# Performance work log

Measured on AMD Instinct MI355X. Metric: run time of the kernel, lower is better.

The kernel has to match this reference:

```python
import jax, jax.numpy as jnp
import numpy as np

N0, N1, N2 = 200000, 50000, 10000
E0, E1 = 800000, 160000
IN_DIM, H1, H2, EMB = 256, 256, 256, 128


def gcn_layer(h_src, src_idx, dst_idx, n_src, n_dst, W, b):
    # DGL GraphConv, norm='both': D_dst^{-1/2} A D_src^{-1/2} X W + b,
    # degrees clamped to min 1 (allow_zero_in_degree=True -> zero rows stay zero).
    ones = jnp.ones(src_idx.shape[0], dtype=h_src.dtype)
    out_deg = jnp.clip(jax.ops.segment_sum(ones, src_idx, num_segments=n_src), 1.0)
    in_deg = jnp.clip(jax.ops.segment_sum(ones, dst_idx, num_segments=n_dst), 1.0)
    # in_dim >= out_dim here, so DGL multiplies by W first then aggregates;
    # result is identical either way.
    h = (h_src * jax.lax.rsqrt(out_deg)[:, None]) @ W          # [n_src, out]
    agg = jax.ops.segment_sum(h[src_idx], dst_idx, num_segments=n_dst)  # [n_dst, out]
    return agg * jax.lax.rsqrt(in_deg)[:, None] + b


def setup_inputs() -> dict:
    key = jax.random.key(0)
    ks = jax.random.split(key, 10)
    h = jax.random.normal(ks[0], (N0, IN_DIM), dtype=jnp.float32)
    src0 = jax.random.randint(ks[1], (E0,), 0, N0, dtype=jnp.int32)
    dst0 = jax.random.randint(ks[2], (E0,), 0, N1, dtype=jnp.int32)
    src1 = jax.random.randint(ks[3], (E1,), 0, N1, dtype=jnp.int32)
    dst1 = jax.random.randint(ks[4], (E1,), 0, N2, dtype=jnp.int32)
    s1 = 1.0 / np.sqrt(IN_DIM)
    s2 = 1.0 / np.sqrt(H1)
    sp = 1.0 / np.sqrt(H2)
    W1 = jax.random.normal(ks[5], (IN_DIM, H1), dtype=jnp.float32) * s1
    W2 = jax.random.normal(ks[6], (H1, H2), dtype=jnp.float32) * s2
    Wp = jax.random.normal(ks[7], (H2, EMB), dtype=jnp.float32) * sp
    b1 = jnp.zeros((H1,), dtype=jnp.float32)
    b2 = jnp.zeros((H2,), dtype=jnp.float32)
    bp = jnp.zeros((EMB,), dtype=jnp.float32)
    return {"h": h, "src0": src0, "dst0": dst0, "src1": src1, "dst1": dst1,
            "W1": W1, "b1": b1, "W2": W2, "b2": b2, "Wp": Wp, "bp": bp}


def reference(h, src0, dst0, src1, dst1, W1, b1, W2, b2, Wp, bp):
    h = gcn_layer(h, src0, dst0, N0, N1, W1, b1)   # [N1, H1]
    h = gcn_layer(h, src1, dst1, N1, N2, W2, b2)   # [N2, H2]
    return h @ Wp + bp                             # [N2, EMB]
```

## Files before the change

### kernel.cpp

```cpp
#include <hip/hip_runtime.h>
#include <cstddef>

#define N0 200000
#define N1 50000
#define N2 10000
#define E0 800000
#define E1 160000

typedef short bf16x8 __attribute__((ext_vector_type(8)));
typedef float f32x4 __attribute__((ext_vector_type(4)));
typedef unsigned short us8 __attribute__((ext_vector_type(8)));

__device__ __forceinline__ unsigned short f2bf(float f) {
    unsigned int u = __float_as_uint(f);
    unsigned int r = (u + 0x7FFF + ((u >> 16) & 1)) >> 16;
    return (unsigned short)r;
}
__device__ __forceinline__ float bf2f(unsigned short s) {
    return __uint_as_float(((unsigned int)s) << 16);
}

__global__ void pack_all(const float* __restrict__ W1, const float* __restrict__ W2,
                         const float* __restrict__ Wp,
                         unsigned short* __restrict__ W1p, unsigned short* __restrict__ W2p,
                         unsigned short* __restrict__ Wpp) {
    int tid = blockIdx.x * 256 + threadIdx.x;
    if (tid >= 320 * 64) return;
    int lane = tid & 63;
    int tile = tid >> 6;
    const float* W; unsigned short* Bp; int N; int lt;
    if (tile < 128)      { W = W1; Bp = W1p; N = 256; lt = tile; }
    else if (tile < 256) { W = W2; Bp = W2p; N = 256; lt = tile - 128; }
    else                 { W = Wp; Bp = Wpp; N = 128; lt = tile - 256; }
    int s  = lt & 7;
    int ct = lt >> 3;
    int col = ct * 16 + (lane & 15);
    int k0  = s * 32 + (lane >> 4) * 8;
    unsigned short* dst = Bp + ((size_t)lt * 64 + lane) * 8;
#pragma unroll
    for (int j = 0; j < 8; j++) dst[j] = f2bf(W[(size_t)(k0 + j) * N + col]);
}

__global__ void count_all(const int* __restrict__ src0, const int* __restrict__ dst0,
                          const int* __restrict__ src1, const int* __restrict__ dst1,
                          int* __restrict__ cnt_out0, int* __restrict__ cnt_in0,
                          int* __restrict__ cnt_out1, int* __restrict__ cnt_in1,
                          int* __restrict__ rank0, int* __restrict__ rank1) {
    int e = blockIdx.x * 256 + threadIdx.x;
    if (e < E0) {
        atomicAdd(&cnt_out0[src0[e]], 1);
        rank0[e] = atomicAdd(&cnt_in0[dst0[e]], 1);
    } else if (e < E0 + E1) {
        int f = e - E0;
        atomicAdd(&cnt_out1[src1[f]], 1);
        rank1[f] = atomicAdd(&cnt_in1[dst1[f]], 1);
    }
}

__global__ __launch_bounds__(256) void prescale_bf16(const float* __restrict__ H,
                                                     const int* __restrict__ cnt_out,
                                                     unsigned short* __restrict__ hsb) {
    const long long total = (long long)N0 * 32;
    const long long stride = (long long)gridDim.x * 256;
    for (long long g = (long long)blockIdx.x * 256 + threadIdx.x; g < total; g += stride) {
        int row = (int)(g >> 5);
        float rs = rsqrtf((float)max(cnt_out[row], 1));
        const float* p = H + g * 8;
        float4 x = *(const float4*)p;
        float4 y = *(const float4*)(p + 4);
        us8 o;
        o[0] = f2bf(x.x * rs); o[1] = f2bf(x.y * rs); o[2] = f2bf(x.z * rs); o[3] = f2bf(x.w * rs);
        o[4] = f2bf(y.x * rs); o[5] = f2bf(y.y * rs); o[6] = f2bf(y.z * rs); o[7] = f2bf(y.w * rs);
        *(us8*)(hsb + g * 8) = o;
    }
}

__global__ void scales_kernel(const int* __restrict__ cnt, float* __restrict__ rs, int n) {
    int i = blockIdx.x * 256 + threadIdx.x;
    if (i < n) rs[i] = rsqrtf((float)max(cnt[i], 1));
}

__global__ __launch_bounds__(1024) void scan2(const int* __restrict__ cnt_in0, int* __restrict__ rowptr0,
                                              const int* __restrict__ cnt_in1, int* __restrict__ rowptr1) {
    const int* cnt = blockIdx.x ? cnt_in1 : cnt_in0;
    int* rowptr    = blockIdx.x ? rowptr1 : rowptr0;
    const int n    = blockIdx.x ? N2 : N1;
    __shared__ int partial[1024];
    const int t = threadIdx.x;
    const int chunk = (n + 1023) / 1024;
    const int begin = t * chunk;
    const int end = min(begin + chunk, n);
    int sum = 0;
    for (int i = begin; i < end; i++) sum += cnt[i];
    partial[t] = sum;
    __syncthreads();
    for (int off = 1; off < 1024; off <<= 1) {
        int v = (t >= off) ? partial[t - off] : 0;
        __syncthreads();
        partial[t] += v;
        __syncthreads();
    }
    int run = partial[t] - sum;
    for (int i = begin; i < end; i++) {
        rowptr[i] = run;
        run += cnt[i];
    }
    if (t == 1023) rowptr[n] = partial[1023];
}

__global__ void fill_all(const int* __restrict__ src0, const int* __restrict__ dst0,
                         const int* __restrict__ src1, const int* __restrict__ dst1,
                         const int* __restrict__ rank0, const int* __restrict__ rank1,
                         const int* __restrict__ rowptr0, const int* __restrict__ rowptr1,
                         int* __restrict__ csr0, int* __restrict__ csr1) {
    int e = blockIdx.x * 256 + threadIdx.x;
    if (e < E0) {
        csr0[rowptr0[dst0[e]] + rank0[e]] = src0[e];
    } else if (e < E0 + E1) {
        int f = e - E0;
        csr1[rowptr1[dst1[f]] + rank1[f]] = src1[f];
    }
}

template <int NT, bool AF32, bool OBF16, bool BS>
__global__ __launch_bounds__(256) void gemm_mfma(const void* __restrict__ A_,
                                                 const unsigned short* __restrict__ Bp,
                                                 const float* __restrict__ rs,
                                                 const float* __restrict__ bias,
                                                 void* __restrict__ C_, int M, int N) {
    const int lane = threadIdx.x & 63;
    const int wave = threadIdx.x >> 6;
    const int rowBase = blockIdx.x * 64 + wave * 16;
    const int lm = lane & 15;
    const int quad = lane >> 4;

    f32x4 acc[NT];
#pragma unroll
    for (int ct = 0; ct < NT; ct++) acc[ct] = (f32x4){0.f, 0.f, 0.f, 0.f};

    const int rowA = min(rowBase + lm, M - 1);
    const float* af32 = (const float*)A_ + (size_t)rowA * 256 + quad * 8;
    const unsigned short* abf = (const unsigned short*)A_ + (size_t)rowA * 256 + quad * 8;

#pragma unroll 2
    for (int s = 0; s < 8; s++) {
        bf16x8 afrag;
        if (AF32) {
            float4 x = *(const float4*)(af32 + s * 32);
            float4 y = *(const float4*)(af32 + s * 32 + 4);
            union { unsigned short u[8]; bf16x8 v; } af;
            af.u[0] = f2bf(x.x); af.u[1] = f2bf(x.y); af.u[2] = f2bf(x.z); af.u[3] = f2bf(x.w);
            af.u[4] = f2bf(y.x); af.u[5] = f2bf(y.y); af.u[6] = f2bf(y.z); af.u[7] = f2bf(y.w);
            afrag = af.v;
        } else {
            afrag = *(const bf16x8*)(abf + s * 32);
        }
#pragma unroll
        for (int ct = 0; ct < NT; ct++) {
            bf16x8 bfrag = *(const bf16x8*)(Bp + (((size_t)ct * 8 + s) * 64 + lane) * 8);
            acc[ct] = __builtin_amdgcn_mfma_f32_16x16x32_bf16(afrag, bfrag, acc[ct], 0, 0, 0);
        }
    }

    f32x4 rsv = (f32x4){1.f, 1.f, 1.f, 1.f};
    if (rs) rsv = *(const f32x4*)(rs + min(rowBase + quad * 4, M - 4));
#pragma unroll
    for (int ct = 0; ct < NT; ct++) {
        int col = ct * 16 + lm;
        float bv = bias ? bias[col] : 0.0f;
#pragma unroll
        for (int i = 0; i < 4; i++) {
            int row = rowBase + quad * 4 + i;
            if (row < M) {
                float v = acc[ct][i];
                if (BS) { v = (v + bv) * rsv[i]; }
                else    { v = v * rsv[i] + bv; }
                if (OBF16) ((unsigned short*)C_)[(size_t)row * N + col] = f2bf(v);
                else       ((float*)C_)[(size_t)row * N + col] = v;
            }
        }
    }
}

__global__ __launch_bounds__(256) void gather_bf16(const unsigned short* __restrict__ Y,
                                                   const int* __restrict__ rowptr,
                                                   const int* __restrict__ csr,
                                                   const float* __restrict__ rs_dst,
                                                   const float* __restrict__ bias,
                                                   unsigned short* __restrict__ outb, int n_dst) {
    int w    = (blockIdx.x * 256 + threadIdx.x) >> 6;
    int lane = threadIdx.x & 63;
    if (w >= n_dst) return;
    int half = lane >> 5;
    int l32  = lane & 31;
    int e   = rowptr[w];
    int end = rowptr[w + 1];
    float acc[8] = {0.f, 0.f, 0.f, 0.f, 0.f, 0.f, 0.f, 0.f};
    for (; e + 7 < end; e += 8) {
        int s0 = csr[e + half];
        int s1 = csr[e + 2 + half];
        int s2 = csr[e + 4 + half];
        int s3 = csr[e + 6 + half];
        us8 v0 = *(const us8*)(Y + (size_t)s0 * 256 + l32 * 8);
        us8 v1 = *(const us8*)(Y + (size_t)s1 * 256 + l32 * 8);
        us8 v2 = *(const us8*)(Y + (size_t)s2 * 256 + l32 * 8);
        us8 v3 = *(const us8*)(Y + (size_t)s3 * 256 + l32 * 8);
#pragma unroll
        for (int j = 0; j < 8; j++)
            acc[j] += (bf2f(v0[j]) + bf2f(v1[j])) + (bf2f(v2[j]) + bf2f(v3[j]));
    }
    for (; e + 1 < end; e += 2) {
        int s0 = csr[e + half];
        us8 v0 = *(const us8*)(Y + (size_t)s0 * 256 + l32 * 8);
#pragma unroll
        for (int j = 0; j < 8; j++) acc[j] += bf2f(v0[j]);
    }
    if (e < end && half == 0) {
        int s0 = csr[e];
        us8 v0 = *(const us8*)(Y + (size_t)s0 * 256 + l32 * 8);
#pragma unroll
        for (int j = 0; j < 8; j++) acc[j] += bf2f(v0[j]);
    }
#pragma unroll
    for (int j = 0; j < 8; j++) acc[j] += __shfl_xor(acc[j], 32);
    if (half == 0) {
        float sd = rs_dst[w];
        float bj[8] = {0.f, 0.f, 0.f, 0.f, 0.f, 0.f, 0.f, 0.f};
        if (bias) {
            f32x4 ba = *(const f32x4*)(bias + l32 * 8);
            f32x4 bb = *(const f32x4*)(bias + l32 * 8 + 4);
            bj[0] = ba[0]; bj[1] = ba[1]; bj[2] = ba[2]; bj[3] = ba[3];
            bj[4] = bb[0]; bj[5] = bb[1]; bj[6] = bb[2]; bj[7] = bb[3];
        }
        us8 o;
#pragma unroll
        for (int j = 0; j < 8; j++) o[j] = f2bf(acc[j] * sd + bj[j]);
        *(us8*)(outb + (size_t)w * 256 + l32 * 8) = o;
    }
}

extern "C" void kernel_launch(void* const* d_in, const int* in_sizes, int n_in,
                              void* d_out, int out_size, void* d_ws, size_t ws_size,
                              hipStream_t stream) {
    const float* h    = (const float*)d_in[0];
    const int*   src0 = (const int*)d_in[1];
    const int*   dst0 = (const int*)d_in[2];
    const int*   src1 = (const int*)d_in[3];
    const int*   dst1 = (const int*)d_in[4];
    const float* W1   = (const float*)d_in[5];
    const float* b1   = (const float*)d_in[6];
    const float* W2   = (const float*)d_in[7];
    const float* b2   = (const float*)d_in[8];
    const float* Wp   = (const float*)d_in[9];
    const float* bp   = (const float*)d_in[10];
    float* out = (float*)d_out;

    int* ib = (int*)d_ws;
    int* cnt_out0 = ib;
    int* cnt_in0  = cnt_out0 + N0;
    int* cnt_out1 = cnt_in0 + N1;
    int* cnt_in1  = cnt_out1 + N1;
    int* rowptr0  = ib + 310000;
    int* rowptr1  = ib + 360001;
    int* csr0     = ib + 370004;
    int* csr1     = ib + 1170004;
    float* fb = (float*)(ib + 1330004);
    float* rs_out0 = fb;
    float* rs_in0  = fb + 200000;
    float* rs_out1 = fb + 250000;
    float* rs_in1  = fb + 300000;
    unsigned short* wpk = (unsigned short*)(fb + 310000);
    unsigned short* W1p = wpk;
    unsigned short* W2p = wpk + 65536;
    unsigned short* Wpp = wpk + 131072;
    unsigned short* R1  = wpk + 163840;
    int* rank0 = (int*)R1;
    int* rank1 = rank0 + E0;
    unsigned short* a0b = R1;
    unsigned short* a1b = R1;
    unsigned short* R3  = R1 + (size_t)N1 * 256;
    unsigned short* hsb = R3;
    unsigned short* t1  = R3;
    unsigned short* h2b = R3 + (size_t)N1 * 256;

    hipMemsetAsync(cnt_out0, 0, (size_t)310000 * sizeof(int), stream);

    pack_all<<<80, 256, 0, stream>>>(W1, W2, Wp, W1p, W2p, Wpp);

    count_all<<<(E0 + E1 + 255) / 256, 256, 0, stream>>>(src0, dst0, src1, dst1,
                                                         cnt_out0, cnt_in0, cnt_out1, cnt_in1,
                                                         rank0, rank1);

    prescale_bf16<<<2048, 256, 0, stream>>>(h, cnt_out0, hsb);

    scales_kernel<<<(310000 + 255) / 256, 256, 0, stream>>>(cnt_out0, rs_out0, 310000);

    scan2<<<2, 1024, 0, stream>>>(cnt_in0, rowptr0, cnt_in1, rowptr1);

    fill_all<<<(E0 + E1 + 255) / 256, 256, 0, stream>>>(src0, dst0, src1, dst1,
                                                        rank0, rank1, rowptr0, rowptr1, csr0, csr1);

    gather_bf16<<<(N1 + 3) / 4, 256, 0, stream>>>(hsb, rowptr0, csr0, rs_in0, nullptr, a0b, N1);

    gemm_mfma<16, false, true, true><<<(N1 + 63) / 64, 256, 0, stream>>>(a0b, W1p, rs_out1, b1, t1, N1, 256);

    gather_bf16<<<(N2 + 3) / 4, 256, 0, stream>>>(t1, rowptr1, csr1, rs_in1, nullptr, a1b, N2);

    gemm_mfma<16, false, true, false><<<(N2 + 63) / 64, 256, 0, stream>>>(a1b, W2p, nullptr, b2, h2b, N2, 256);

    gemm_mfma<8, false, false, false><<<(N2 + 63) / 64, 256, 0, stream>>>(h2b, Wpp, nullptr, bp, out, N2, 128);
}
```

Before: 662.1 us.

## Build CSR with atomic cursors, trim scales pass, deepen gather unroll

The per-edge rank arrays are dropped. CSR fill now claims slots with an atomicAdd on rowptr, so each rowptr entry ends up at its row's end and the gather reads the row start from rowptr[w-1]. The scales kernel now covers only the in-degree and layer-1 out-degree counts, because the layer-0 out-degree scale is already computed inline in prescale. The gather loop gains a 16-edge unrolled stage with more loads in flight, and its unused bias path is removed. The cost is extra atomic contention during fill and a nondeterministic edge order within each row, which changes the order of floating-point summation.

```diff
diff --git a/kernel.cpp b/kernel.cpp
--- a/kernel.cpp
+++ b/kernel.cpp
@@ -44,16 +44,15 @@
 __global__ void count_all(const int* __restrict__ src0, const int* __restrict__ dst0,
                           const int* __restrict__ src1, const int* __restrict__ dst1,
                           int* __restrict__ cnt_out0, int* __restrict__ cnt_in0,
-                          int* __restrict__ cnt_out1, int* __restrict__ cnt_in1,
-                          int* __restrict__ rank0, int* __restrict__ rank1) {
+                          int* __restrict__ cnt_out1, int* __restrict__ cnt_in1) {
     int e = blockIdx.x * 256 + threadIdx.x;
     if (e < E0) {
         atomicAdd(&cnt_out0[src0[e]], 1);
-        rank0[e] = atomicAdd(&cnt_in0[dst0[e]], 1);
+        atomicAdd(&cnt_in0[dst0[e]], 1);
     } else if (e < E0 + E1) {
         int f = e - E0;
         atomicAdd(&cnt_out1[src1[f]], 1);
-        rank1[f] = atomicAdd(&cnt_in1[dst1[f]], 1);
+        atomicAdd(&cnt_in1[dst1[f]], 1);
     }
 }
 
@@ -110,15 +109,14 @@
 
 __global__ void fill_all(const int* __restrict__ src0, const int* __restrict__ dst0,
                          const int* __restrict__ src1, const int* __restrict__ dst1,
-                         const int* __restrict__ rank0, const int* __restrict__ rank1,
-                         const int* __restrict__ rowptr0, const int* __restrict__ rowptr1,
+                         int* __restrict__ rowptr0, int* __restrict__ rowptr1,
                          int* __restrict__ csr0, int* __restrict__ csr1) {
     int e = blockIdx.x * 256 + threadIdx.x;
     if (e < E0) {
-        csr0[rowptr0[dst0[e]] + rank0[e]] = src0[e];
+        csr0[atomicAdd(&rowptr0[dst0[e]], 1)] = src0[e];
     } else if (e < E0 + E1) {
         int f = e - E0;
-        csr1[rowptr1[dst1[f]] + rank1[f]] = src1[f];
+        csr1[atomicAdd(&rowptr1[dst1[f]], 1)] = src1[f];
     }
 }
 
@@ -186,16 +184,37 @@
                                                    const int* __restrict__ rowptr,
                                                    const int* __restrict__ csr,
                                                    const float* __restrict__ rs_dst,
-                                                   const float* __restrict__ bias,
                                                    unsigned short* __restrict__ outb, int n_dst) {
     int w    = (blockIdx.x * 256 + threadIdx.x) >> 6;
     int lane = threadIdx.x & 63;
     if (w >= n_dst) return;
     int half = lane >> 5;
     int l32  = lane & 31;
-    int e   = rowptr[w];
-    int end = rowptr[w + 1];
+    int e   = (w == 0) ? 0 : rowptr[w - 1];
+    int end = rowptr[w];
     float acc[8] = {0.f, 0.f, 0.f, 0.f, 0.f, 0.f, 0.f, 0.f};
+    for (; e + 15 < end; e += 16) {
+        int s0 = csr[e + half];
+        int s1 = csr[e + 2 + half];
+        int s2 = csr[e + 4 + half];
+        int s3 = csr[e + 6 + half];
+        int s4 = csr[e + 8 + half];
+        int s5 = csr[e + 10 + half];
+        int s6 = csr[e + 12 + half];
+        int s7 = csr[e + 14 + half];
+        us8 v0 = *(const us8*)(Y + (size_t)s0 * 256 + l32 * 8);
+        us8 v1 = *(const us8*)(Y + (size_t)s1 * 256 + l32 * 8);
+        us8 v2 = *(const us8*)(Y + (size_t)s2 * 256 + l32 * 8);
+        us8 v3 = *(const us8*)(Y + (size_t)s3 * 256 + l32 * 8);
+        us8 v4 = *(const us8*)(Y + (size_t)s4 * 256 + l32 * 8);
+        us8 v5 = *(const us8*)(Y + (size_t)s5 * 256 + l32 * 8);
+        us8 v6 = *(const us8*)(Y + (size_t)s6 * 256 + l32 * 8);
+        us8 v7 = *(const us8*)(Y + (size_t)s7 * 256 + l32 * 8);
+#pragma unroll
+        for (int j = 0; j < 8; j++)
+            acc[j] += ((bf2f(v0[j]) + bf2f(v1[j])) + (bf2f(v2[j]) + bf2f(v3[j])))
+                    + ((bf2f(v4[j]) + bf2f(v5[j])) + (bf2f(v6[j]) + bf2f(v7[j])));
+    }
     for (; e + 7 < end; e += 8) {
         int s0 = csr[e + half];
         int s1 = csr[e + 2 + half];
@@ -225,16 +244,9 @@
     for (int j = 0; j < 8; j++) acc[j] += __shfl_xor(acc[j], 32);
     if (half == 0) {
         float sd = rs_dst[w];
-        float bj[8] = {0.f, 0.f, 0.f, 0.f, 0.f, 0.f, 0.f, 0.f};
-        if (bias) {
-            f32x4 ba = *(const f32x4*)(bias + l32 * 8);
-            f32x4 bb = *(const f32x4*)(bias + l32 * 8 + 4);
-            bj[0] = ba[0]; bj[1] = ba[1]; bj[2] = ba[2]; bj[3] = ba[3];
-            bj[4] = bb[0]; bj[5] = bb[1]; bj[6] = bb[2]; bj[7] = bb[3];
-        }
         us8 o;
 #pragma unroll
-        for (int j = 0; j < 8; j++) o[j] = f2bf(acc[j] * sd + bj[j]);
+        for (int j = 0; j < 8; j++) o[j] = f2bf(acc[j] * sd);
         *(us8*)(outb + (size_t)w * 256 + l32 * 8) = o;
     }
 }
@@ -274,8 +286,6 @@
     unsigned short* W2p = wpk + 65536;
     unsigned short* Wpp = wpk + 131072;
     unsigned short* R1  = wpk + 163840;
-    int* rank0 = (int*)R1;
-    int* rank1 = rank0 + E0;
     unsigned short* a0b = R1;
     unsigned short* a1b = R1;
     unsigned short* R3  = R1 + (size_t)N1 * 256;
@@ -288,23 +298,22 @@
     pack_all<<<80, 256, 0, stream>>>(W1, W2, Wp, W1p, W2p, Wpp);
 
     count_all<<<(E0 + E1 + 255) / 256, 256, 0, stream>>>(src0, dst0, src1, dst1,
-                                                         cnt_out0, cnt_in0, cnt_out1, cnt_in1,
-                                                         rank0, rank1);
+                                                         cnt_out0, cnt_in0, cnt_out1, cnt_in1);
 
     prescale_bf16<<<2048, 256, 0, stream>>>(h, cnt_out0, hsb);
 
-    scales_kernel<<<(310000 + 255) / 256, 256, 0, stream>>>(cnt_out0, rs_out0, 310000);
+    scales_kernel<<<(110000 + 255) / 256, 256, 0, stream>>>(cnt_in0, rs_in0, 110000);
 
     scan2<<<2, 1024, 0, stream>>>(cnt_in0, rowptr0, cnt_in1, rowptr1);
 
     fill_all<<<(E0 + E1 + 255) / 256, 256, 0, stream>>>(src0, dst0, src1, dst1,
-                                                        rank0, rank1, rowptr0, rowptr1, csr0, csr1);
-
-    gather_bf16<<<(N1 + 3) / 4, 256, 0, stream>>>(hsb, rowptr0, csr0, rs_in0, nullptr, a0b, N1);
+                                                        rowptr0, rowptr1, csr0, csr1);
+
+    gather_bf16<<<(N1 + 3) / 4, 256, 0, stream>>>(hsb, rowptr0, csr0, rs_in0, a0b, N1);
 
     gemm_mfma<16, false, true, true><<<(N1 + 63) / 64, 256, 0, stream>>>(a0b, W1p, rs_out1, b1, t1, N1, 256);
 
-    gather_bf16<<<(N2 + 3) / 4, 256, 0, stream>>>(t1, rowptr1, csr1, rs_in1, nullptr, a1b, N2);
+    gather_bf16<<<(N2 + 3) / 4, 256, 0, stream>>>(t1, rowptr1, csr1, rs_in1, a1b, N2);
 
     gemm_mfma<16, false, true, false><<<(N2 + 63) / 64, 256, 0, stream>>>(a1b, W2p, nullptr, b2, h2b, N2, 256);
 
```

Measured after the change: 695.1 us. +5.0%, slower.
